# Performance work log

Measured on AMD Instinct MI355X. Metric: run time of the kernel, lower is better.

The kernel has to match this reference:

```python
import jax, jax.numpy as jnp
import numpy as np
import math

HEADS = 2
DH = 64
INNER = HEADS * DH  # 128
TOPK = 128
ALPHA = 10.0
N_FREQ = 8  # feature_dim // (2*input_dim) = 64 // 8
OMEGAS = jnp.logspace(1.0, math.log10(128.0), N_FREQ)           # sigma_q = 128
OMEGAS_L = [jnp.logspace(1.0, math.log10(s), N_FREQ) for s in (128.0, 32.0)]
LAYER_NUM = 2


def calc_gamma(grid, omegas):
    # grid: (Q, 4) -> (Q, 4*2*n_freq)
    arg = jnp.pi * grid[:, :, None] * omegas[None, None, :]      # (Q,4,n)
    g = jnp.concatenate([jnp.sin(arg), jnp.cos(arg)], axis=-1)   # (Q,4,2n)
    return g.reshape(grid.shape[0], -1)


def setup_inputs() -> dict:
    key = jax.random.key(0)
    ks = jax.random.split(key, 20)
    B, Q, L, HD, FD, OD = 2, 4096, 1024, 256, 64, 1

    def w(k, shape, fan_in):
        return jax.random.normal(k, shape, dtype=jnp.float32) * (1.0 / np.sqrt(fan_in))

    inp = {
        'x': jax.random.uniform(ks[0], (B, Q, 4), dtype=jnp.float32),
        'tokens': jax.random.normal(ks[1], (B, L, HD), dtype=jnp.float32),
        'query_W': w(ks[2], (FD, HD), FD),
        'query_b': jnp.zeros((HD,), jnp.float32),
        'q_W': w(ks[3], (HD, INNER), HD),
        'kv_W': w(ks[4], (HD, 2 * INNER), HD),
        'out_W': w(ks[5], (INNER, HD), INNER),
        'out_b': jnp.zeros((HD,), jnp.float32),
        'band_W': w(ks[6], (LAYER_NUM, FD, HD), FD),
        'band_b': jnp.zeros((LAYER_NUM, HD), jnp.float32),
        'mod_W': w(ks[7], (LAYER_NUM, HD, HD), HD),
        'mod_b': jnp.zeros((LAYER_NUM, HD), jnp.float32),
        'hv_W': w(ks[8], (LAYER_NUM - 1, HD, HD), HD),
        'hv_b': jnp.zeros((LAYER_NUM - 1, HD), jnp.float32),
        'outl_W': w(ks[9], (LAYER_NUM, HD, OD), HD),
        'outl_b': jnp.zeros((LAYER_NUM, OD), jnp.float32),
        'gD': 8, 'gH': 8, 'gW': 8, 'gT': 8,
    }
    return inp


def reference(x, tokens, query_W, query_b, q_W, kv_W, out_W, out_b,
              band_W, band_b, mod_W, mod_b, hv_W, hv_b, outl_W, outl_b,
              gD, gH, gW, gT):
    B, Q, _ = x.shape
    L = tokens.shape[1]
    grid = x[0]  # (Q, 4) — torch code uses x[0] for all batches

    # --- patch index + approximate relative distances -> sparse attn indices ---
    z_i = (grid[:, 0] * gD).astype(jnp.int32)
    y_i = (grid[:, 1] * gH).astype(jnp.int32)
    x_i = (grid[:, 2] * gW).astype(jnp.int32)
    t_i = (grid[:, 3] * gT).astype(jnp.int32)
    idx = ((t_i * gD + z_i) * gH + y_i) * gW + x_i               # (Q,)
    N = gD * gH * gW * gT
    t = idx / N                                                  # (Q,) float
    tok_pos = (jnp.arange(L, dtype=jnp.float32) + 0.5) / L       # (L,)
    bias = ALPHA * (t[:, None] - tok_pos[None, :]) ** 2          # (Q, L)
    # top-k SMALLEST distances (identical across batch, compute once)
    _, attn_idx = jax.lax.top_k(-bias, TOPK)                     # (Q, k)

    # --- query features ---
    gamma_q = calc_gamma(grid, OMEGAS)                           # (Q, 64)
    x_q = jax.nn.relu(gamma_q @ query_W + query_b)               # (Q, 256)
    x_q = jnp.broadcast_to(x_q[None], (B, Q, x_q.shape[-1]))

    # --- sparse shared-token cross attention ---
    scale = DH ** -0.5
    q = (x_q @ q_W).reshape(B, Q, HEADS, DH)                     # (B,Q,H,Dh)
    kv = tokens @ kv_W                                           # (B,L,2*inner)
    k_full, v_full = kv[..., :INNER], kv[..., INNER:]            # (B,L,inner)
    k_sp = k_full[:, attn_idx, :].reshape(B, Q, TOPK, HEADS, DH)  # (B,Q,k,H,Dh)
    v_sp = v_full[:, attn_idx, :].reshape(B, Q, TOPK, HEADS, DH)
    sim = jnp.einsum('bqhd,bqkhd->bhqk', q, k_sp) * scale        # (B,H,Q,k)
    attn = jax.nn.softmax(sim, axis=-1)
    o = jnp.einsum('bhqk,bqkhd->bqhd', attn, v_sp).reshape(B, Q, INNER)
    modulation = o @ out_W + out_b                               # (B,Q,256)

    # --- per-band modulation ---
    mods = []
    for l in range(LAYER_NUM):
        gamma_l = calc_gamma(grid, OMEGAS_L[l])                  # (Q, 64)
        h_l = jax.nn.relu(gamma_l @ band_W[l] + band_b[l])       # (Q, 256)
        m_l = jax.nn.relu(h_l[None] + modulation @ mod_W[l] + mod_b[l])
        mods.append(m_l)

    h_v = [mods[0]]
    for i in range(LAYER_NUM - 1):
        h_v.append(jax.nn.relu((mods[i + 1] + h_v[i]) @ hv_W[i] + hv_b[i]))

    out = sum(h_v[i] @ outl_W[i] + outl_b[i] for i in range(LAYER_NUM))
    return out  # (B, Q, output_dim)
```

## Files before the change

kernel.cpp:

```cpp
#include <hip/hip_runtime.h>
#include <math.h>

#define BN     2
#define QN     4096
#define LN     1024
#define TOPKN  128
#define PI_F   3.14159265358979323846f

#define LOG2R0 0.52543879f
#define LOG2R1 0.23972456f

#define NCMAX  384
#define PFP    388

typedef __attribute__((ext_vector_type(8))) short  s16x8;
typedef __attribute__((ext_vector_type(4))) short  s16x4;
typedef __attribute__((ext_vector_type(4))) float  f32x4;
typedef unsigned short u16;

__device__ __forceinline__ u16 f2bf(float f) {
    unsigned int u = __float_as_uint(f);
    u = (u + 0x7FFFu + ((u >> 16) & 1u)) >> 16;
    return (u16)u;
}

__device__ __forceinline__ s16x8 ldB(const float* __restrict__ base, int stride) {
    s16x8 r;
    #pragma unroll
    for (int jj = 0; jj < 8; jj++) r[jj] = (short)f2bf(base[(size_t)jj * stride]);
    return r;
}

__device__ __forceinline__ size_t wtile(int n, int k, int K) {
    return (size_t)((n >> 4) * (K >> 5) + (k >> 5)) * 512 + (n & 15) * 32 + (k & 31);
}
__device__ __forceinline__ size_t kidx(int b, int l, int d) {
    return (((size_t)(b * 64 + (l >> 4)) * 16 + (d >> 3)) * 16 + (l & 15)) * 8 + (d & 7);
}
__device__ __forceinline__ size_t vidx(int b, int n, int k) {
    return (((size_t)(b * 8 + (n >> 4)) * 128 + (k >> 3)) * 16 + (n & 15)) * 8 + (k & 7);
}

struct KvS { u16 tok[32 * 264]; };
struct QS  { float shx[128]; u16 gam[32 * 72]; u16 xq[32 * 264]; };
struct TrS { float tile[8][32][33]; };
struct SoS { int hist[1024]; int cur[1024]; };
union PrepS { KvS kv; QS q; TrS tr; SoS so; };

__global__ __launch_bounds__(1024) void prep_kernel(
    const float* __restrict__ tokens, const float* __restrict__ kv_W,
    const float* __restrict__ x, const float* __restrict__ query_W,
    const float* __restrict__ query_b, const float* __restrict__ q_W,
    const float* __restrict__ outW, const float* __restrict__ bandW,
    const float* __restrict__ modW, const float* __restrict__ hvW,
    const int* __restrict__ gDp, const int* __restrict__ gHp,
    const int* __restrict__ gWp, const int* __restrict__ gTp,
    u16* __restrict__ qall, u16* __restrict__ kbf, u16* __restrict__ vtbf,
    u16* __restrict__ outT, u16* __restrict__ bandT,
    u16* __restrict__ modT, u16* __restrict__ hvT,
    int* __restrict__ perm, int* __restrict__ ssort)
{
    __shared__ __align__(16) PrepS sm;
    const int bid = blockIdx.x;
    const int t   = threadIdx.x;
    const int wid = t >> 6, lane = t & 63;
    const int quad = lane >> 4, l16 = lane & 15;

    if (bid < 64) {
        int l0 = bid * 32;
        int b = l0 >> 10, lloc = l0 & 1023;
        #pragma unroll
        for (int i = 0; i < 8; i++) {
            int idx = i * 1024 + t; int row = idx >> 8, col = idx & 255;
            sm.kv.tok[row * 264 + col] = f2bf(tokens[(size_t)(l0 + row) * 256 + col]);
        }
        __syncthreads();
        int m0 = (wid & 1) * 16;
        int c0 = (wid >> 1) * 32;
        f32x4 acc[2];
        acc[0] = (f32x4){0.f, 0.f, 0.f, 0.f};
        acc[1] = (f32x4){0.f, 0.f, 0.f, 0.f};
        for (int kc = 0; kc < 8; kc++) {
            s16x8 a = *(const s16x8*)&sm.kv.tok[(m0 + l16) * 264 + kc * 32 + quad * 8];
            #pragma unroll
            for (int sub = 0; sub < 2; sub++) {
                s16x8 bfr = ldB(&kv_W[(size_t)(kc * 32 + quad * 8) * 256 + c0 + sub * 16 + l16], 256);
                acc[sub] = __builtin_amdgcn_mfma_f32_16x16x32_bf16(a, bfr, acc[sub], 0, 0, 0);
            }
        }
        #pragma unroll
        for (int sub = 0; sub < 2; sub++) {
            int col = c0 + sub * 16 + l16;
            if (col < 128) {
                #pragma unroll
                for (int r = 0; r < 4; r++)
                    kbf[kidx(b, lloc + m0 + quad * 4 + r, col)] = f2bf(acc[sub][r]);
            } else {
                s16x4 pk;
                pk[0] = (short)f2bf(acc[sub][0]); pk[1] = (short)f2bf(acc[sub][1]);
                pk[2] = (short)f2bf(acc[sub][2]); pk[3] = (short)f2bf(acc[sub][3]);
                *(s16x4*)&vtbf[vidx(b, col - 128, lloc + m0 + quad * 4)] = pk;
            }
        }
    } else if (bid < 192) {
        int p0 = (bid - 64) * 32;
        if (t < 128) sm.q.shx[t] = x[p0 * 4 + t];
        __syncthreads();
        #pragma unroll
        for (int j = 0; j < 2; j++) {
            int e = t * 2 + j;
            int g = e >> 6, f = e & 63;
            int c = f >> 4, jj = f & 15, oi = jj & 7;
            float om = 10.0f * exp2f((float)oi * LOG2R0);
            float arg = PI_F * sm.q.shx[g * 4 + c] * om;
            sm.q.gam[g * 72 + f] = f2bf((jj < 8) ? __sinf(arg) : __cosf(arg));
        }
        __syncthreads();
        int m0 = (wid & 1) * 16;
        {
            int c0 = (wid >> 1) * 32;
            f32x4 acc[2];
            acc[0] = (f32x4){0.f, 0.f, 0.f, 0.f};
            acc[1] = (f32x4){0.f, 0.f, 0.f, 0.f};
            for (int kc = 0; kc < 2; kc++) {
                s16x8 a = *(const s16x8*)&sm.q.gam[(m0 + l16) * 72 + kc * 32 + quad * 8];
                #pragma unroll
                for (int sub = 0; sub < 2; sub++) {
                    s16x8 bfr = ldB(&query_W[(size_t)(kc * 32 + quad * 8) * 256 + c0 + sub * 16 + l16], 256);
                    acc[sub] = __builtin_amdgcn_mfma_f32_16x16x32_bf16(a, bfr, acc[sub], 0, 0, 0);
                }
            }
            #pragma unroll
            for (int sub = 0; sub < 2; sub++) {
                int col = c0 + sub * 16 + l16;
                float bias = query_b[col];
                #pragma unroll
                for (int r = 0; r < 4; r++)
                    sm.q.xq[(m0 + quad * 4 + r) * 264 + col] = f2bf(fmaxf(acc[sub][r] + bias, 0.f));
            }
        }
        __syncthreads();
        {
            int n0q = (wid >> 1) * 16;
            f32x4 acc2 = (f32x4){0.f, 0.f, 0.f, 0.f};
            for (int kc = 0; kc < 8; kc++) {
                s16x8 a = *(const s16x8*)&sm.q.xq[(m0 + l16) * 264 + kc * 32 + quad * 8];
                s16x8 bfr = ldB(&q_W[(size_t)(kc * 32 + quad * 8) * 128 + n0q + l16], 128);
                acc2 = __builtin_amdgcn_mfma_f32_16x16x32_bf16(a, bfr, acc2, 0, 0, 0);
            }
            #pragma unroll
            for (int r = 0; r < 4; r++)
                qall[(size_t)(p0 + m0 + quad * 4 + r) * 128 + n0q + l16] = f2bf(acc2[r]);
        }
    } else if (bid < 224) {
        int base = (bid - 192) * 8;
        int tx = t & 31, ty = (t >> 5) & 31;
        #pragma unroll
        for (int it = 0; it < 8; it++) {
            int lt_g = base + it;
            const float* src; int K, lt;
            if (lt_g < 32)       { src = outW;  K = 128; lt = lt_g; }
            else if (lt_g < 64)  { src = bandW; K = 128; lt = lt_g - 32; }
            else if (lt_g < 192) { src = modW;  K = 512; lt = lt_g - 64; }
            else                 { src = hvW;   K = 256; lt = lt_g - 192; }
            int tk = K >> 5;
            int k0 = (lt % tk) * 32, n0 = (lt / tk) * 32;
            sm.tr.tile[it][ty][tx] = src[(size_t)(k0 + ty) * 256 + n0 + tx];
        }
        __syncthreads();
        #pragma unroll
        for (int it = 0; it < 8; it++) {
            int lt_g = base + it;
            u16* dst; int K, lt;
            if (lt_g < 32)       { dst = outT;  K = 128; lt = lt_g; }
            else if (lt_g < 64)  { dst = bandT; K = 128; lt = lt_g - 32; }
            else if (lt_g < 192) { dst = modT;  K = 512; lt = lt_g - 64; }
            else                 { dst = hvT;   K = 256; lt = lt_g - 192; }
            int tk = K >> 5;
            int k0 = (lt % tk) * 32, n0 = (lt / tk) * 32;
            dst[wtile(n0 + ty, k0 + tx, K)] = f2bf(sm.tr.tile[it][tx][ty]);
        }
    } else {
        int gD = gDp[0], gH = gHp[0], gW = gWp[0], gT = gTp[0];
        int Ng = gD * gH * gW * gT;
        sm.so.hist[t] = 0;
        __syncthreads();
        int sarr[4];
        #pragma unroll
        for (int i = 0; i < 4; i++) {
            int q = i * 1024 + t;
            float4 xv = *(const float4*)&x[q * 4];
            int zi = (int)(xv.x * (float)gD);
            int yi = (int)(xv.y * (float)gH);
            int xi = (int)(xv.z * (float)gW);
            int ti = (int)(xv.w * (float)gT);
            int idx = ((ti * gD + zi) * gH + yi) * gW + xi;
            float tt = (float)idx / (float)Ng;
            int s = (int)ceilf(tt * (float)LN - ((float)(TOPKN / 2) + 0.5f));
            s = min(max(s, 0), LN - TOPKN);
            sarr[i] = s;
            atomicAdd(&sm.so.hist[s], 1);
        }
        __syncthreads();
        int cnt = sm.so.hist[t];
        int incl = cnt;
        #pragma unroll
        for (int off = 1; off < 64; off <<= 1) {
            int u = __shfl_up(incl, off);
            if (lane >= off) incl += u;
        }
        if (lane == 63) sm.so.cur[wid] = incl;
        __syncthreads();
        if (wid == 0) {
            int v = (lane < 16) ? sm.so.cur[lane] : 0;
            #pragma unroll
            for (int off = 1; off < 16; off <<= 1) {
                int u = __shfl_up(v, off);
                if (lane >= off) v += u;
            }
            if (lane < 16) sm.so.cur[lane] = v;
        }
        __syncthreads();
        int woff = wid ? sm.so.cur[wid - 1] : 0;
        sm.so.hist[t] = woff + incl - cnt;
        __syncthreads();
        #pragma unroll
        for (int i = 0; i < 4; i++) {
            int q = i * 1024 + t;
            int pos = atomicAdd(&sm.so.hist[sarr[i]], 1);
            perm[pos] = q;
            ssort[pos] = sarr[i];
        }
    }
}

__global__ __launch_bounds__(1024, 4) void fused_kernel(
    const float* __restrict__ x,
    const u16* __restrict__ kbf, const u16* __restrict__ vtbf,
    const u16* __restrict__ qall,
    const int* __restrict__ perm, const int* __restrict__ ssort,
    const u16* __restrict__ outT, const float* __restrict__ out_b,
    const u16* __restrict__ bandT, const float* __restrict__ band_b,
    const u16* __restrict__ modT, const float* __restrict__ mod_b,
    const u16* __restrict__ hvT, const float* __restrict__ hv_b,
    const float* __restrict__ outl_W, const float* __restrict__ outl_b,
    float* __restrict__ out)
{
    const int bid = blockIdx.x;
    const int b   = bid >> 7;
    const int g0  = (bid & 127) * 32;
    const int t   = threadIdx.x;
    const int wid = t >> 6, lane = t & 63;
    const int quad = lane >> 4, l16 = lane & 15;

    __shared__ __align__(16) u16 q_bf[32 * 136];
    __shared__ __align__(16) u16 gam_lds[64 * 72];
    __shared__ __align__(16) float scores32[64 * PFP];
    __shared__ __align__(16) u16 o_lds[32 * 136];
    __shared__ float fin[16 * 32];
    __shared__ float sh_xc[128];
    __shared__ int sh_pq[32], sh_s[32];

    u16* modu_lds = (u16*)scores32;
    u16* s01_lds  = ((u16*)scores32) + 32 * 264;

    if (t < 32) { sh_pq[t] = perm[g0 + t]; sh_s[t] = ssort[g0 + t]; }
    __syncthreads();

    {
        int m = t >> 5, d = (t & 31) * 4;
        *(uint2*)&q_bf[m * 136 + d] = *(const uint2*)&qall[(size_t)sh_pq[m] * 128 + d];
    }
    if (t < 128) sh_xc[t] = x[(size_t)sh_pq[t >> 2] * 4 + (t & 3)];
    __syncthreads();

    #pragma unroll
    for (int j = 0; j < 4; j++) {
        int e = j * 1024 + t;
        int l = e >> 11, g = (e >> 6) & 31, f = e & 63;
        int c = f >> 4, jj = f & 15, oi = jj & 7;
        float om = 10.0f * exp2f((float)oi * (l ? LOG2R1 : LOG2R0));
        float arg = PI_F * sh_xc[g * 4 + c] * om;
        gam_lds[(l * 32 + g) * 72 + f] = f2bf((jj < 8) ? __sinf(arg) : __cosf(arg));
    }

    const int u0    = sh_s[0] & ~15;
    const int ncols = min((sh_s[31] + 128 - u0 + 31) & ~31, NCMAX);
    const int nsub  = ncols >> 4;
    const int nkc   = ncols >> 5;

    {
        s16x8 aq[2][4];
        #pragma unroll
        for (int rh = 0; rh < 2; rh++)
            #pragma unroll
            for (int c = 0; c < 4; c++)
                aq[rh][c] = *(const s16x8*)&q_bf[(rh * 16 + l16) * 136 + c * 32 + quad * 8];
        for (int j = wid; j < 2 * nsub; j += 16) {
            int h = (j >= nsub) ? 1 : 0;
            int sub = j - h * nsub;
            int lrow = u0 + sub * 16 + l16;
            f32x4 acc0 = (f32x4){0.f, 0.f, 0.f, 0.f};
            f32x4 acc1 = (f32x4){0.f, 0.f, 0.f, 0.f};
            s16x8 b0 = *(const s16x8*)&kbf[kidx(b, lrow, h * 64 + quad * 8)];
            s16x8 b1 = *(const s16x8*)&kbf[kidx(b, lrow, h * 64 + 32 + quad * 8)];
            acc0 = __builtin_amdgcn_mfma_f32_16x16x32_bf16(aq[0][h * 2 + 0], b0, acc0, 0, 0, 0);
            acc0 = __builtin_amdgcn_mfma_f32_16x16x32_bf16(aq[0][h * 2 + 1], b1, acc0, 0, 0, 0);
            acc1 = __builtin_amdgcn_mfma_f32_16x16x32_bf16(aq[1][h * 2 + 0], b0, acc1, 0, 0, 0);
            acc1 = __builtin_amdgcn_mfma_f32_16x16x32_bf16(aq[1][h * 2 + 1], b1, acc1, 0, 0, 0);
            #pragma unroll
            for (int r = 0; r < 4; r++) {
                scores32[(h * 32 + quad * 4 + r) * PFP + sub * 16 + l16] = acc0[r];
                scores32[(h * 32 + 16 + quad * 4 + r) * PFP + sub * 16 + l16] = acc1[r];
            }
        }
    }
    __syncthreads();

    {
        #pragma unroll
        for (int rr = 0; rr < 4; rr++) {
            int row = wid + rr * 16;
            int qq  = row & 31;
            int sg  = sh_s[qq];
            float vals[6]; int ok[6];
            float mx = -1e30f;
            #pragma unroll
            for (int i = 0; i < 6; i++) {
                int c = lane + 64 * i;
                float v = scores32[row * PFP + c] * 0.125f;
                int key = u0 + c;
                int o2 = (c < ncols) && (key >= sg) && (key < sg + 128);
                vals[i] = v; ok[i] = o2;
                if (o2) mx = fmaxf(mx, v);
            }
            #pragma unroll
            for (int off = 1; off < 64; off <<= 1) mx = fmaxf(mx, __shfl_xor(mx, off));
            float sum = 0.f, e6[6];
            #pragma unroll
            for (int i = 0; i < 6; i++) {
                float e = ok[i] ? __expf(vals[i] - mx) : 0.f;
                e6[i] = e; sum += e;
            }
            #pragma unroll
            for (int off = 1; off < 64; off <<= 1) sum += __shfl_xor(sum, off);
            float inv = 1.f / sum;
            u16* prow = (u16*)&scores32[row * PFP];
            #pragma unroll
            for (int i = 0; i < 6; i++) {
                int c = lane + 64 * i;
                if (c < ncols) prow[c] = f2bf(e6[i] * inv);
            }
        }
    }
    __syncthreads();

    {
        int ct = wid & 7, rh = wid >> 3;
        int h = ct >> 2;
        const u16* prow = (const u16*)&scores32[(h * 32 + rh * 16 + l16) * PFP];
        f32x4 acc = (f32x4){0.f, 0.f, 0.f, 0.f};
        #pragma unroll 2
        for (int kc = 0; kc < nkc; kc++) {
            s16x8 a = *(const s16x8*)&prow[kc * 32 + quad * 8];
            int koff = u0 + kc * 32 + quad * 8;
            koff = min(koff, 1016);
            s16x8 bfr = *(const s16x8*)&vtbf[vidx(b, ct * 16 + l16, koff)];
            acc = __builtin_amdgcn_mfma_f32_16x16x32_bf16(a, bfr, acc, 0, 0, 0);
        }
        #pragma unroll
        for (int r = 0; r < 4; r++)
            o_lds[(rh * 16 + quad * 4 + r) * 136 + ct * 16 + l16] = f2bf(acc[r]);
    }
    __syncthreads();

    const int n0 = wid * 16;
    float m0f[2][4];

    {
        f32x4 am0 = (f32x4){0.f, 0.f, 0.f, 0.f};
        f32x4 am1 = (f32x4){0.f, 0.f, 0.f, 0.f};
        #pragma unroll
        for (int kc = 0; kc < 4; kc++) {
            s16x8 bfr = *(const s16x8*)&outT[wtile(n0 + l16, kc * 32 + quad * 8, 128)];
            s16x8 a0 = *(const s16x8*)&o_lds[l16 * 136 + kc * 32 + quad * 8];
            s16x8 a1 = *(const s16x8*)&o_lds[(16 + l16) * 136 + kc * 32 + quad * 8];
            am0 = __builtin_amdgcn_mfma_f32_16x16x32_bf16(a0, bfr, am0, 0, 0, 0);
            am1 = __builtin_amdgcn_mfma_f32_16x16x32_bf16(a1, bfr, am1, 0, 0, 0);
        }
        int col = n0 + l16;
        float bias = out_b[col];
        #pragma unroll
        for (int r = 0; r < 4; r++) {
            modu_lds[(quad * 4 + r) * 264 + col] = f2bf(am0[r] + bias);
            modu_lds[(16 + quad * 4 + r) * 264 + col] = f2bf(am1[r] + bias);
        }
    }
    __syncthreads();

    #pragma unroll
    for (int l = 0; l < 2; l++) {
        f32x4 ab0 = (f32x4){0.f, 0.f, 0.f, 0.f};
        f32x4 ab1 = (f32x4){0.f, 0.f, 0.f, 0.f};
        f32x4 am0 = (f32x4){0.f, 0.f, 0.f, 0.f};
        f32x4 am1 = (f32x4){0.f, 0.f, 0.f, 0.f};
        #pragma unroll
        for (int kc = 0; kc < 2; kc++) {
            s16x8 bfr = *(const s16x8*)&bandT[wtile(n0 + l16, l * 64 + kc * 32 + quad * 8, 128)];
            s16x8 a0 = *(const s16x8*)&gam_lds[(l * 32 + l16) * 72 + kc * 32 + quad * 8];
            s16x8 a1 = *(const s16x8*)&gam_lds[(l * 32 + 16 + l16) * 72 + kc * 32 + quad * 8];
            ab0 = __builtin_amdgcn_mfma_f32_16x16x32_bf16(a0, bfr, ab0, 0, 0, 0);
            ab1 = __builtin_amdgcn_mfma_f32_16x16x32_bf16(a1, bfr, ab1, 0, 0, 0);
        }
        #pragma unroll
        for (int kc = 0; kc < 8; kc++) {
            s16x8 bfr = *(const s16x8*)&modT[wtile(n0 + l16, l * 256 + kc * 32 + quad * 8, 512)];
            s16x8 a0 = *(const s16x8*)&modu_lds[l16 * 264 + kc * 32 + quad * 8];
            s16x8 a1 = *(const s16x8*)&modu_lds[(16 + l16) * 264 + kc * 32 + quad * 8];
            am0 = __builtin_amdgcn_mfma_f32_16x16x32_bf16(a0, bfr, am0, 0, 0, 0);
            am1 = __builtin_amdgcn_mfma_f32_16x16x32_bf16(a1, bfr, am1, 0, 0, 0);
        }
        int col = n0 + l16;
        float bb = band_b[l * 256 + col];
        float mb = mod_b[l * 256 + col];
        #pragma unroll
        for (int r = 0; r < 4; r++) {
            float h0 = fmaxf(ab0[r] + bb, 0.f);
            float v0 = fmaxf(h0 + am0[r] + mb, 0.f);
            float h1 = fmaxf(ab1[r] + bb, 0.f);
            float v1 = fmaxf(h1 + am1[r] + mb, 0.f);
            if (l == 0) { m0f[0][r] = v0; m0f[1][r] = v1; }
            else {
                s01_lds[(quad * 4 + r) * 264 + col] = f2bf(m0f[0][r] + v0);
                s01_lds[(16 + quad * 4 + r) * 264 + col] = f2bf(m0f[1][r] + v1);
            }
        }
    }
    __syncthreads();

    {
        f32x4 ah0 = (f32x4){0.f, 0.f, 0.f, 0.f};
        f32x4 ah1 = (f32x4){0.f, 0.f, 0.f, 0.f};
        #pragma unroll
        for (int kc = 0; kc < 8; kc++) {
            s16x8 bfr = *(const s16x8*)&hvT[wtile(n0 + l16, kc * 32 + quad * 8, 256)];
            s16x8 a0 = *(const s16x8*)&s01_lds[l16 * 264 + kc * 32 + quad * 8];
            s16x8 a1 = *(const s16x8*)&s01_lds[(16 + l16) * 264 + kc * 32 + quad * 8];
            ah0 = __builtin_amdgcn_mfma_f32_16x16x32_bf16(a0, bfr, ah0, 0, 0, 0);
            ah1 = __builtin_amdgcn_mfma_f32_16x16x32_bf16(a1, bfr, ah1, 0, 0, 0);
        }
        int col = n0 + l16;
        float w0 = outl_W[col], w1 = outl_W[256 + col], hb = hv_b[col];
        #pragma unroll
        for (int r = 0; r < 4; r++) {
            float pv0 = m0f[0][r] * w0 + fmaxf(ah0[r] + hb, 0.f) * w1;
            float pv1 = m0f[1][r] * w0 + fmaxf(ah1[r] + hb, 0.f) * w1;
            #pragma unroll
            for (int off = 1; off < 16; off <<= 1) {
                pv0 += __shfl_xor(pv0, off);
                pv1 += __shfl_xor(pv1, off);
            }
            if (l16 == 0) {
                fin[wid * 32 + quad * 4 + r] = pv0;
                fin[wid * 32 + 16 + quad * 4 + r] = pv1;
            }
        }
    }
    __syncthreads();
    if (t < 32) {
        float s2 = outl_b[0] + outl_b[1];
        #pragma unroll
        for (int w = 0; w < 16; w++) s2 += fin[w * 32 + t];
        out[(size_t)b * QN + sh_pq[t]] = s2;
    }
}

extern "C" void kernel_launch(void* const* d_in, const int* in_sizes, int n_in,
                              void* d_out, int out_size, void* d_ws, size_t ws_size,
                              hipStream_t stream)
{
    const float* x       = (const float*)d_in[0];
    const float* tokens  = (const float*)d_in[1];
    const float* query_W = (const float*)d_in[2];
    const float* query_b = (const float*)d_in[3];
    const float* q_W     = (const float*)d_in[4];
    const float* kv_W    = (const float*)d_in[5];
    const float* out_W   = (const float*)d_in[6];
    const float* out_b   = (const float*)d_in[7];
    const float* band_W  = (const float*)d_in[8];
    const float* band_b  = (const float*)d_in[9];
    const float* mod_W   = (const float*)d_in[10];
    const float* mod_b   = (const float*)d_in[11];
    const float* hv_W    = (const float*)d_in[12];
    const float* hv_b    = (const float*)d_in[13];
    const float* outl_W  = (const float*)d_in[14];
    const float* outl_b  = (const float*)d_in[15];
    const int*   gD      = (const int*)d_in[16];
    const int*   gH      = (const int*)d_in[17];
    const int*   gW      = (const int*)d_in[18];
    const int*   gT      = (const int*)d_in[19];

    float* ws   = (float*)d_ws;
    u16* qall   = (u16*)ws;
    u16* wb = (u16*)(ws + 524288);
    u16* kbf   = wb;
    u16* vtbf  = wb + 262144;
    u16* outT  = wb + 524288;
    u16* bandT = wb + 557056;
    u16* modT  = wb + 589824;
    u16* hvT   = wb + 720896;
    int* perm  = (int*)(wb + 786432);
    int* ssort = perm + 4096;
    float* out = (float*)d_out;

    prep_kernel<<<225, 1024, 0, stream>>>(tokens, kv_W, x, query_W, query_b, q_W,
                                          out_W, band_W, mod_W, hv_W,
                                          gD, gH, gW, gT,
                                          qall, kbf, vtbf, outT, bandT, modT, hvT,
                                          perm, ssort);
    fused_kernel<<<256, 1024, 0, stream>>>(x, kbf, vtbf, qall, perm, ssort,
        outT, out_b, bandT, band_b, modT, mod_b, hvT, hv_b,
        outl_W, outl_b, out);
}
```

Before: 121.6 us.

## Prefetch K, V and weight fragments into registers ahead of dependent stages

Global loads are issued early so their latency overlaps earlier work. The first K tile, the first six V chunks, the out-projection weights and the band weights are loaded into registers before the stages that need them, while the gamma features, scores and softmax are still being computed. The band GEMM also moves earlier, next to the out-projection. To allow a fixed six-step unrolled PV loop, the softmax now writes probabilities for all columns, relying on zeros past ncols. The cost is much higher VGPR pressure, which can lower occupancy or cause spills.

```diff
diff --git a/kernel.cpp b/kernel.cpp
--- a/kernel.cpp
+++ b/kernel.cpp
@@ -267,6 +267,24 @@
     if (t < 32) { sh_pq[t] = perm[g0 + t]; sh_s[t] = ssort[g0 + t]; }
     __syncthreads();
 
+    const int u0    = sh_s[0] & ~15;
+    const int ncols = min((sh_s[31] + 128 - u0 + 31) & ~31, NCMAX);
+    const int nsub  = ncols >> 4;
+    const int nkc   = ncols >> 5;
+
+    const int ct = wid & 7, rh = wid >> 3;
+    s16x8 vf[6];
+    #pragma unroll
+    for (int kc = 0; kc < 6; kc++) {
+        int koff = min(u0 + kc * 32 + quad * 8, 1016);
+        vf[kc] = *(const s16x8*)&vtbf[vidx(b, ct * 16 + l16, koff)];
+    }
+    const int h1   = (wid >= nsub) ? 1 : 0;
+    const int sub1 = wid - h1 * nsub;
+    const int lrow1 = u0 + sub1 * 16 + l16;
+    s16x8 kb0 = *(const s16x8*)&kbf[kidx(b, lrow1, h1 * 64 + quad * 8)];
+    s16x8 kb1 = *(const s16x8*)&kbf[kidx(b, lrow1, h1 * 64 + 32 + quad * 8)];
+
     {
         int m = t >> 5, d = (t & 31) * 4;
         *(uint2*)&q_bf[m * 136 + d] = *(const uint2*)&qall[(size_t)sh_pq[m] * 128 + d];
@@ -284,19 +302,27 @@
         gam_lds[(l * 32 + g) * 72 + f] = f2bf((jj < 8) ? __sinf(arg) : __cosf(arg));
     }
 
-    const int u0    = sh_s[0] & ~15;
-    const int ncols = min((sh_s[31] + 128 - u0 + 31) & ~31, NCMAX);
-    const int nsub  = ncols >> 4;
-    const int nkc   = ncols >> 5;
-
     {
         s16x8 aq[2][4];
         #pragma unroll
-        for (int rh = 0; rh < 2; rh++)
+        for (int rh2 = 0; rh2 < 2; rh2++)
             #pragma unroll
             for (int c = 0; c < 4; c++)
-                aq[rh][c] = *(const s16x8*)&q_bf[(rh * 16 + l16) * 136 + c * 32 + quad * 8];
-        for (int j = wid; j < 2 * nsub; j += 16) {
+                aq[rh2][c] = *(const s16x8*)&q_bf[(rh2 * 16 + l16) * 136 + c * 32 + quad * 8];
+        {
+            f32x4 acc0 = (f32x4){0.f, 0.f, 0.f, 0.f};
+            f32x4 acc1 = (f32x4){0.f, 0.f, 0.f, 0.f};
+            acc0 = __builtin_amdgcn_mfma_f32_16x16x32_bf16(aq[0][h1 * 2 + 0], kb0, acc0, 0, 0, 0);
+            acc0 = __builtin_amdgcn_mfma_f32_16x16x32_bf16(aq[0][h1 * 2 + 1], kb1, acc0, 0, 0, 0);
+            acc1 = __builtin_amdgcn_mfma_f32_16x16x32_bf16(aq[1][h1 * 2 + 0], kb0, acc1, 0, 0, 0);
+            acc1 = __builtin_amdgcn_mfma_f32_16x16x32_bf16(aq[1][h1 * 2 + 1], kb1, acc1, 0, 0, 0);
+            #pragma unroll
+            for (int r = 0; r < 4; r++) {
+                scores32[(h1 * 32 + quad * 4 + r) * PFP + sub1 * 16 + l16] = acc0[r];
+                scores32[(h1 * 32 + 16 + quad * 4 + r) * PFP + sub1 * 16 + l16] = acc1[r];
+            }
+        }
+        for (int j = wid + 16; j < 2 * nsub; j += 16) {
             int h = (j >= nsub) ? 1 : 0;
             int sub = j - h * nsub;
             int lrow = u0 + sub * 16 + l16;
@@ -349,22 +375,30 @@
             #pragma unroll
             for (int i = 0; i < 6; i++) {
                 int c = lane + 64 * i;
-                if (c < ncols) prow[c] = f2bf(e6[i] * inv);
-            }
-        }
-    }
-    __syncthreads();
+                prow[c] = f2bf(e6[i] * inv);
+            }
+        }
+    }
+    __syncthreads();
+
+    const int n0 = wid * 16;
+    s16x8 wout[4];
+    #pragma unroll
+    for (int kc = 0; kc < 4; kc++)
+        wout[kc] = *(const s16x8*)&outT[wtile(n0 + l16, kc * 32 + quad * 8, 128)];
 
     {
-        int ct = wid & 7, rh = wid >> 3;
-        int h = ct >> 2;
-        const u16* prow = (const u16*)&scores32[(h * 32 + rh * 16 + l16) * PFP];
+        int hh = ct >> 2;
+        const u16* prow = (const u16*)&scores32[(hh * 32 + rh * 16 + l16) * PFP];
         f32x4 acc = (f32x4){0.f, 0.f, 0.f, 0.f};
-        #pragma unroll 2
-        for (int kc = 0; kc < nkc; kc++) {
+        #pragma unroll
+        for (int kc = 0; kc < 6; kc++) {
             s16x8 a = *(const s16x8*)&prow[kc * 32 + quad * 8];
-            int koff = u0 + kc * 32 + quad * 8;
-            koff = min(koff, 1016);
+            acc = __builtin_amdgcn_mfma_f32_16x16x32_bf16(a, vf[kc], acc, 0, 0, 0);
+        }
+        for (int kc = 6; kc < nkc; kc++) {
+            s16x8 a = *(const s16x8*)&prow[kc * 32 + quad * 8];
+            int koff = min(u0 + kc * 32 + quad * 8, 1016);
             s16x8 bfr = *(const s16x8*)&vtbf[vidx(b, ct * 16 + l16, koff)];
             acc = __builtin_amdgcn_mfma_f32_16x16x32_bf16(a, bfr, acc, 0, 0, 0);
         }
@@ -374,19 +408,35 @@
     }
     __syncthreads();
 
-    const int n0 = wid * 16;
-    float m0f[2][4];
-
+    f32x4 ab[2][2];
     {
+        s16x8 wband[4];
+        #pragma unroll
+        for (int l = 0; l < 2; l++)
+            #pragma unroll
+            for (int kc = 0; kc < 2; kc++)
+                wband[l * 2 + kc] = *(const s16x8*)&bandT[wtile(n0 + l16, l * 64 + kc * 32 + quad * 8, 128)];
+
         f32x4 am0 = (f32x4){0.f, 0.f, 0.f, 0.f};
         f32x4 am1 = (f32x4){0.f, 0.f, 0.f, 0.f};
         #pragma unroll
         for (int kc = 0; kc < 4; kc++) {
-            s16x8 bfr = *(const s16x8*)&outT[wtile(n0 + l16, kc * 32 + quad * 8, 128)];
             s16x8 a0 = *(const s16x8*)&o_lds[l16 * 136 + kc * 32 + quad * 8];
             s16x8 a1 = *(const s16x8*)&o_lds[(16 + l16) * 136 + kc * 32 + quad * 8];
-            am0 = __builtin_amdgcn_mfma_f32_16x16x32_bf16(a0, bfr, am0, 0, 0, 0);
-            am1 = __builtin_amdgcn_mfma_f32_16x16x32_bf16(a1, bfr, am1, 0, 0, 0);
+            am0 = __builtin_amdgcn_mfma_f32_16x16x32_bf16(a0, wout[kc], am0, 0, 0, 0);
+            am1 = __builtin_amdgcn_mfma_f32_16x16x32_bf16(a1, wout[kc], am1, 0, 0, 0);
+        }
+        #pragma unroll
+        for (int l = 0; l < 2; l++) {
+            ab[l][0] = (f32x4){0.f, 0.f, 0.f, 0.f};
+            ab[l][1] = (f32x4){0.f, 0.f, 0.f, 0.f};
+            #pragma unroll
+            for (int kc = 0; kc < 2; kc++) {
+                s16x8 a0 = *(const s16x8*)&gam_lds[(l * 32 + l16) * 72 + kc * 32 + quad * 8];
+                s16x8 a1 = *(const s16x8*)&gam_lds[(l * 32 + 16 + l16) * 72 + kc * 32 + quad * 8];
+                ab[l][0] = __builtin_amdgcn_mfma_f32_16x16x32_bf16(a0, wband[l * 2 + kc], ab[l][0], 0, 0, 0);
+                ab[l][1] = __builtin_amdgcn_mfma_f32_16x16x32_bf16(a1, wband[l * 2 + kc], ab[l][1], 0, 0, 0);
+            }
         }
         int col = n0 + l16;
         float bias = out_b[col];
@@ -398,37 +448,28 @@
     }
     __syncthreads();
 
+    float m0f[2][4];
     #pragma unroll
     for (int l = 0; l < 2; l++) {
-        f32x4 ab0 = (f32x4){0.f, 0.f, 0.f, 0.f};
-        f32x4 ab1 = (f32x4){0.f, 0.f, 0.f, 0.f};
-        f32x4 am0 = (f32x4){0.f, 0.f, 0.f, 0.f};
-        f32x4 am1 = (f32x4){0.f, 0.f, 0.f, 0.f};
-        #pragma unroll
-        for (int kc = 0; kc < 2; kc++) {
-            s16x8 bfr = *(const s16x8*)&bandT[wtile(n0 + l16, l * 64 + kc * 32 + quad * 8, 128)];
-            s16x8 a0 = *(const s16x8*)&gam_lds[(l * 32 + l16) * 72 + kc * 32 + quad * 8];
-            s16x8 a1 = *(const s16x8*)&gam_lds[(l * 32 + 16 + l16) * 72 + kc * 32 + quad * 8];
-            ab0 = __builtin_amdgcn_mfma_f32_16x16x32_bf16(a0, bfr, ab0, 0, 0, 0);
-            ab1 = __builtin_amdgcn_mfma_f32_16x16x32_bf16(a1, bfr, ab1, 0, 0, 0);
-        }
+        f32x4 amod0 = (f32x4){0.f, 0.f, 0.f, 0.f};
+        f32x4 amod1 = (f32x4){0.f, 0.f, 0.f, 0.f};
         #pragma unroll
         for (int kc = 0; kc < 8; kc++) {
             s16x8 bfr = *(const s16x8*)&modT[wtile(n0 + l16, l * 256 + kc * 32 + quad * 8, 512)];
             s16x8 a0 = *(const s16x8*)&modu_lds[l16 * 264 + kc * 32 + quad * 8];
             s16x8 a1 = *(const s16x8*)&modu_lds[(16 + l16) * 264 + kc * 32 + quad * 8];
-            am0 = __builtin_amdgcn_mfma_f32_16x16x32_bf16(a0, bfr, am0, 0, 0, 0);
-            am1 = __builtin_amdgcn_mfma_f32_16x16x32_bf16(a1, bfr, am1, 0, 0, 0);
+            amod0 = __builtin_amdgcn_mfma_f32_16x16x32_bf16(a0, bfr, amod0, 0, 0, 0);
+            amod1 = __builtin_amdgcn_mfma_f32_16x16x32_bf16(a1, bfr, amod1, 0, 0, 0);
         }
         int col = n0 + l16;
         float bb = band_b[l * 256 + col];
         float mb = mod_b[l * 256 + col];
         #pragma unroll
         for (int r = 0; r < 4; r++) {
-            float h0 = fmaxf(ab0[r] + bb, 0.f);
-            float v0 = fmaxf(h0 + am0[r] + mb, 0.f);
-            float h1 = fmaxf(ab1[r] + bb, 0.f);
-            float v1 = fmaxf(h1 + am1[r] + mb, 0.f);
+            float h0 = fmaxf(ab[l][0][r] + bb, 0.f);
+            float v0 = fmaxf(h0 + amod0[r] + mb, 0.f);
+            float h1 = fmaxf(ab[l][1][r] + bb, 0.f);
+            float v1 = fmaxf(h1 + amod1[r] + mb, 0.f);
             if (l == 0) { m0f[0][r] = v0; m0f[1][r] = v1; }
             else {
                 s01_lds[(quad * 4 + r) * 264 + col] = f2bf(m0f[0][r] + v0);
```

After: 120.0 us. No clear change (-1.3%).
